# Kernel tuning notes

Measured on AMD Instinct MI355X. Metric: run time of the kernel, lower is better.

The kernel has to match this reference:

```python
import jax, jax.numpy as jnp
import numpy as np

DIMS = 512
NUM_HEADS = 8
KEY_DIM = DIMS // NUM_HEADS  # 64
VAL_DIM = DIMS               # 512, shared across heads
B, L = 4, 2048


def setup_inputs() -> dict:
    key = jax.random.key(0)
    ks = jax.random.split(key, 13)
    s = 0.02
    return {
        "query": jax.random.normal(ks[0], (B, L, DIMS), dtype=jnp.float32),
        "key": jax.random.normal(ks[1], (B, L, DIMS), dtype=jnp.float32),
        "value": jax.random.normal(ks[2], (B, L, DIMS), dtype=jnp.float32),
        # linear weights stored as (in, out)
        "Wq": jax.random.normal(ks[3], (DIMS, KEY_DIM * NUM_HEADS), dtype=jnp.float32) * s,
        "bq": jnp.zeros((KEY_DIM * NUM_HEADS,), dtype=jnp.float32),
        "Wk": jax.random.normal(ks[4], (DIMS, KEY_DIM * NUM_HEADS), dtype=jnp.float32) * s,
        "bk": jnp.zeros((KEY_DIM * NUM_HEADS,), dtype=jnp.float32),
        "Wv": jax.random.normal(ks[5], (DIMS, VAL_DIM), dtype=jnp.float32) * s,
        "bv": jnp.zeros((VAL_DIM,), dtype=jnp.float32),
        "Wo": jax.random.normal(ks[6], (VAL_DIM * NUM_HEADS, DIMS), dtype=jnp.float32) * s,
        "bo": jnp.zeros((DIMS,), dtype=jnp.float32),
    }


def reference(query, key, value, Wq, bq, Wk, bk, Wv, bv, Wo, bo):
    b, l, _ = query.shape
    m = key.shape[1]
    q = (query @ Wq + bq).reshape(b, l, KEY_DIM, NUM_HEADS)   # blkh
    k = (key @ Wk + bk).reshape(b, m, KEY_DIM, NUM_HEADS)     # bmkh
    v = value @ Wv + bv                                        # bmv (shared over heads)
    # causal mask: -inf strictly above the diagonal
    mask = jnp.where(jnp.arange(m)[None, :] > jnp.arange(l)[:, None],
                     jnp.float32(-jnp.inf), jnp.float32(0.0))  # [l, m]
    scores = jnp.einsum('blkh,bmkh->bhlm', q, k) + mask
    # original divides (scores+mask) by sqrt(key_dim) before softmax
    attn = jax.nn.softmax(scores / jnp.sqrt(jnp.float32(KEY_DIM)), axis=-1)
    vals = jnp.einsum('bhlm,bmv->blhv', attn, v).reshape(b, l, NUM_HEADS * VAL_DIM)
    return vals @ Wo + bo
```

## Files before the change

kernel.cpp:

```cpp
#include <hip/hip_runtime.h>
#include <hip/hip_bf16.h>


typedef __attribute__((ext_vector_type(8))) short bf16x8;
typedef __attribute__((ext_vector_type(4))) float f32x4;
typedef unsigned short u16;
typedef unsigned int u32;

#define DIMS  512
#define NHEAD 8
#define KDIM  64
#define VDIM  512
#define BATCH 4
#define SEQ   2048
#define ROWS  (BATCH * SEQ)
#define OCOLS (NHEAD * VDIM)

__device__ __forceinline__ u16 f2bf(float x) {
  __hip_bfloat16 b = __float2bfloat16(x);
  u16 u; __builtin_memcpy(&u, &b, 2); return u;
}
__device__ __forceinline__ float bf2f(u16 u) {
  __hip_bfloat16 b; __builtin_memcpy(&b, &u, 2); return __bfloat162float(b);
}

__global__ __launch_bounds__(256) void cast_bf16(
    const float* __restrict__ in, u16* __restrict__ out, int n8) {
  int i = blockIdx.x * 256 + threadIdx.x;
  if (i >= n8) return;
  const float4* p = reinterpret_cast<const float4*>(in) + (size_t)i * 2;
  float4 a0 = p[0], a1 = p[1];
  bf16x8 v;
  v[0] = f2bf(a0.x); v[1] = f2bf(a0.y); v[2] = f2bf(a0.z); v[3] = f2bf(a0.w);
  v[4] = f2bf(a1.x); v[5] = f2bf(a1.y); v[6] = f2bf(a1.z); v[7] = f2bf(a1.w);
  reinterpret_cast<bf16x8*>(out)[i] = v;
}

__global__ __launch_bounds__(256) void transpose_to_bf16(
    const float* __restrict__ in, u16* __restrict__ out, int R, int C) {
  __shared__ float t[32][33];
  int tx = threadIdx.x & 31, ty = threadIdx.x >> 5;
  int r0 = blockIdx.y * 32, c0 = blockIdx.x * 32;
  #pragma unroll
  for (int i = 0; i < 32; i += 8)
    t[ty + i][tx] = in[(size_t)(r0 + ty + i) * C + c0 + tx];
  __syncthreads();
  #pragma unroll
  for (int i = 0; i < 32; i += 8) {
    int oc = ty + i;
    out[(size_t)(c0 + oc) * R + r0 + tx] = f2bf(t[tx][oc]);
  }
}

__global__ __launch_bounds__(256) void proj_kernel(
    const u16* __restrict__ Xb, const u16* __restrict__ Wt,
    const float* __restrict__ bias, u16* __restrict__ out,
    int mode, float scale) {
  __shared__ u16 Ct[64][72];
  int lane = threadIdx.x & 63, wave = threadIdx.x >> 6;
  int g = lane >> 4, l15 = lane & 15;
  int row0 = blockIdx.y * 64, cb = blockIdx.x * 64;
  int gr = row0 + wave * 16 + l15;
  f32x4 acc[4] = {};
  for (int k0 = 0; k0 < DIMS; k0 += 32) {
    int ka = k0 + g * 8;
    bf16x8 a = *reinterpret_cast<const bf16x8*>(Xb + (size_t)gr * DIMS + ka);
    #pragma unroll
    for (int c = 0; c < 4; ++c) {
      bf16x8 bfr = *reinterpret_cast<const bf16x8*>(Wt + (size_t)(cb + c * 16 + l15) * DIMS + ka);
      acc[c] = __builtin_amdgcn_mfma_f32_16x16x32_bf16(a, bfr, acc[c], 0, 0, 0);
    }
  }
  #pragma unroll
  for (int c = 0; c < 4; ++c) {
    int col = c * 16 + l15;
    float bi = bias[cb + col];
    #pragma unroll
    for (int r = 0; r < 4; ++r) {
      int rl = wave * 16 + g * 4 + r;
      float v = (acc[c][r] + bi) * scale;
      if (mode == 0) Ct[rl][col] = f2bf(v);
      else           Ct[col][rl] = f2bf(v);
    }
  }
  __syncthreads();
  if (mode == 0) {
    int kd0 = cb >> 3;
    #pragma unroll
    for (int s2 = 0; s2 < 2; ++s2) {
      int seg = threadIdx.x + s2 * 256;
      int l = seg >> 3, h = seg & 7;
      bf16x8 vp;
      #pragma unroll
      for (int j = 0; j < 8; ++j) vp[j] = (short)Ct[l][h + 8 * j];
      int row = row0 + l;
      int b = row >> 11, ll = row & 2047;
      *reinterpret_cast<bf16x8*>(out + (((size_t)(b * NHEAD + h) * SEQ + ll) * KDIM + kd0)) = vp;
    }
  } else {
    int v_ = threadIdx.x >> 2, ch = threadIdx.x & 3;
    int b = row0 >> 11, m0 = row0 & 2047;
    bf16x8 p0, p1;
    #pragma unroll
    for (int j = 0; j < 8; ++j) { p0[j] = (short)Ct[v_][ch * 16 + j]; p1[j] = (short)Ct[v_][ch * 16 + 8 + j]; }
    u16* dst = out + ((size_t)(b * VDIM + cb + v_)) * SEQ + m0 + ch * 16;
    *reinterpret_cast<bf16x8*>(dst) = p0;
    *reinterpret_cast<bf16x8*>(dst + 8) = p1;
  }
}

__global__ __launch_bounds__(256, 3) void attn_kernel(
    const u16* __restrict__ Qp, const u16* __restrict__ Kp,
    const u16* __restrict__ Vt, u16* __restrict__ vals) {
  __shared__ char P[4][4096];
  int lane = threadIdx.x & 63, wave = threadIdx.x >> 6;
  int g = lane >> 4, l15 = lane & 15;
  int wg = blockIdx.x;
  int xcd = wg & 7, idx = wg >> 3;
  int bh = xcd * 4 + (idx & 3);
  int qt = 63 - (idx >> 2);
  int b = bh >> 3, h = bh & 7;
  int q0 = qt * 32;
  const u16* Qh = Qp + (size_t)bh * SEQ * KDIM;
  const u16* Kh = Kp + (size_t)bh * SEQ * KDIM;
  const u16* Vw = Vt + (size_t)b * VDIM * SEQ + (size_t)(wave * 128) * SEQ;
  char* Pw = P[wave];

  bf16x8 qb[2][2];
  #pragma unroll
  for (int rf = 0; rf < 2; ++rf)
    #pragma unroll
    for (int ks = 0; ks < 2; ++ks)
      qb[rf][ks] = *reinterpret_cast<const bf16x8*>(
          Qh + (size_t)(q0 + rf * 16 + l15) * KDIM + ks * 32 + g * 8);

  f32x4 acc[2][8] = {};
  float rs[2] = {0.f, 0.f};
  int nt = (qt >> 1) + 1;
  int nfull = (qt * 32 + 1) >> 6;

  auto tile = [&](int t, bool masked) {
    int m0 = t * 64;
    #pragma unroll
    for (int hf = 0; hf < 2; ++hf) {
      bf16x8 ka[2][2];
      #pragma unroll
      for (int i = 0; i < 2; ++i)
        #pragma unroll
        for (int ks = 0; ks < 2; ++ks)
          ka[i][ks] = *reinterpret_cast<const bf16x8*>(
              Kh + (size_t)(m0 + (hf * 2 + i) * 16 + l15) * KDIM + ks * 32 + g * 8);
      f32x4 st[2][2] = {};
      #pragma unroll
      for (int ks = 0; ks < 2; ++ks)
        #pragma unroll
        for (int i = 0; i < 2; ++i)
          #pragma unroll
          for (int rf = 0; rf < 2; ++rf)
            st[i][rf] = __builtin_amdgcn_mfma_f32_16x16x32_bf16(ka[i][ks], qb[rf][ks], st[i][rf], 0, 0, 0);
      #pragma unroll
      for (int i = 0; i < 2; ++i) {
        int mb = hf * 2 + i;
        int mbase = m0 + mb * 16 + g * 4;
        #pragma unroll
        for (int rf = 0; rf < 2; ++rf) {
          int qv = q0 + rf * 16 + l15;
          u16 pb[4];
          #pragma unroll
          for (int r = 0; r < 4; ++r) {
            float p = (masked && (mbase + r > qv)) ? 0.f : exp2f(st[i][rf][r]);
            pb[r] = f2bf(p);
            rs[rf] += bf2f(pb[r]);
          }
          uint2 w;
          w.x = (u32)pb[0] | ((u32)pb[1] << 16);
          w.y = (u32)pb[2] | ((u32)pb[3] << 16);
          int row = rf * 16 + l15;
          int byt = row * 128 + ((mb * 32 + g * 8) ^ ((row & 7) << 4));
          *reinterpret_cast<uint2*>(Pw + byt) = w;
        }
      }
    }
    #pragma unroll
    for (int ks = 0; ks < 2; ++ks) {
      bf16x8 pa[2];
      #pragma unroll
      for (int ar = 0; ar < 2; ++ar) {
        int row = ar * 16 + l15;
        pa[ar] = *reinterpret_cast<const bf16x8*>(
            Pw + row * 128 + ((ks * 64 + g * 16) ^ ((row & 7) << 4)));
      }
      #pragma unroll
      for (int c = 0; c < 8; ++c) {
        bf16x8 vb = *reinterpret_cast<const bf16x8*>(
            Vw + (size_t)(c * 16 + l15) * SEQ + m0 + ks * 32 + g * 8);
        #pragma unroll
        for (int ar = 0; ar < 2; ++ar)
          acc[ar][c] = __builtin_amdgcn_mfma_f32_16x16x32_bf16(pa[ar], vb, acc[ar][c], 0, 0, 0);
      }
    }
  };

  for (int t = 0; t < nfull; ++t) tile(t, false);
  for (int t = nfull; t < nt; ++t) tile(t, true);

  #pragma unroll
  for (int rf = 0; rf < 2; ++rf) {
    float v = rs[rf];
    v += __shfl_xor(v, 16);
    v += __shfl_xor(v, 32);
    rs[rf] = 1.0f / v;
  }
  float rinv[2][4];
  #pragma unroll
  for (int ar = 0; ar < 2; ++ar)
    #pragma unroll
    for (int r = 0; r < 4; ++r)
      rinv[ar][r] = __shfl(rs[ar], (lane & 48) | (((lane >> 4) & 3) * 4 + r));

  #pragma unroll
  for (int ar = 0; ar < 2; ++ar) {
    #pragma unroll
    for (int c = 0; c < 8; ++c) {
      int vcol = wave * 128 + c * 16 + l15;
      #pragma unroll
      for (int r = 0; r < 4; ++r) {
        int row = ar * 16 + g * 4 + r;
        float o = acc[ar][c][r] * rinv[ar][r];
        vals[((size_t)(b * SEQ + q0 + row)) * OCOLS + h * VDIM + vcol] = f2bf(o);
      }
    }
  }
}

__global__ __launch_bounds__(256) void out_gemm(
    const u16* __restrict__ vals, const u16* __restrict__ Wot,
    const float* __restrict__ bo, float* __restrict__ out) {
  __shared__ char As[128 * 128];
  __shared__ char Bs[64 * 128];
  int t = threadIdx.x;
  int lane = t & 63, wave = t >> 6;
  int g = lane >> 4, l15 = lane & 15;
  int id = (blockIdx.x & 7) * 64 + (blockIdx.x >> 3);
  int bx = id & 7, by = id >> 3;
  int row0 = by * 128, col0 = bx * 64;
  const int NT = OCOLS / 64;

  auto aglob = [&](int kt, int i) {
    int cid = t + i * 256, r = cid >> 3, ch = cid & 7;
    return *reinterpret_cast<const bf16x8*>(vals + (size_t)(row0 + r) * OCOLS + kt * 64 + ch * 8);
  };
  auto bglob = [&](int kt, int i) {
    int cid = t + i * 256, r = cid >> 3, ch = cid & 7;
    return *reinterpret_cast<const bf16x8*>(Wot + (size_t)(col0 + r) * OCOLS + kt * 64 + ch * 8);
  };
  auto stash = [&](bf16x8* av, bf16x8* bv) {
    #pragma unroll
    for (int i = 0; i < 4; ++i) {
      int cid = t + i * 256, r = cid >> 3, ch = cid & 7;
      *reinterpret_cast<bf16x8*>(As + r * 128 + ((ch * 16) ^ ((r & 7) << 4))) = av[i];
    }
    #pragma unroll
    for (int i = 0; i < 2; ++i) {
      int cid = t + i * 256, r = cid >> 3, ch = cid & 7;
      *reinterpret_cast<bf16x8*>(Bs + r * 128 + ((ch * 16) ^ ((r & 7) << 4))) = bv[i];
    }
  };

  f32x4 acc[2][4] = {};
  bf16x8 av[4], bv[2];
  #pragma unroll
  for (int i = 0; i < 4; ++i) av[i] = aglob(0, i);
  #pragma unroll
  for (int i = 0; i < 2; ++i) bv[i] = bglob(0, i);
  stash(av, bv);
  __syncthreads();

  for (int kt = 0; kt < NT; ++kt) {
    bf16x8 an[4], bn[2];
    if (kt + 1 < NT) {
      #pragma unroll
      for (int i = 0; i < 4; ++i) an[i] = aglob(kt + 1, i);
      #pragma unroll
      for (int i = 0; i < 2; ++i) bn[i] = bglob(kt + 1, i);
    }
    #pragma unroll
    for (int ks = 0; ks < 2; ++ks) {
      bf16x8 af[2];
      #pragma unroll
      for (int rf = 0; rf < 2; ++rf) {
        int row = wave * 32 + rf * 16 + l15;
        af[rf] = *reinterpret_cast<const bf16x8*>(As + row * 128 + ((ks * 64 + g * 16) ^ ((row & 7) << 4)));
      }
      #pragma unroll
      for (int c = 0; c < 4; ++c) {
        int row = c * 16 + l15;
        bf16x8 bfr = *reinterpret_cast<const bf16x8*>(Bs + row * 128 + ((ks * 64 + g * 16) ^ ((row & 7) << 4)));
        #pragma unroll
        for (int rf = 0; rf < 2; ++rf)
          acc[rf][c] = __builtin_amdgcn_mfma_f32_16x16x32_bf16(af[rf], bfr, acc[rf][c], 0, 0, 0);
      }
    }
    __syncthreads();
    if (kt + 1 < NT) {
      stash(an, bn);
      __syncthreads();
    }
  }

  #pragma unroll
  for (int c = 0; c < 4; ++c) {
    int col = col0 + c * 16 + l15;
    float bi = bo[col];
    #pragma unroll
    for (int rf = 0; rf < 2; ++rf)
      #pragma unroll
      for (int r = 0; r < 4; ++r) {
        int row = row0 + wave * 32 + rf * 16 + g * 4 + r;
        out[(size_t)row * DIMS + col] = acc[rf][c][r] + bi;
      }
  }
}

extern "C" void kernel_launch(void* const* d_in, const int* in_sizes, int n_in,
                              void* d_out, int out_size, void* d_ws, size_t ws_size,
                              hipStream_t stream) {
  const float* query = (const float*)d_in[0];
  const float* key   = (const float*)d_in[1];
  const float* value = (const float*)d_in[2];
  const float* Wq    = (const float*)d_in[3];
  const float* bq    = (const float*)d_in[4];
  const float* Wk    = (const float*)d_in[5];
  const float* bk    = (const float*)d_in[6];
  const float* Wv    = (const float*)d_in[7];
  const float* bv    = (const float*)d_in[8];
  const float* Wo    = (const float*)d_in[9];
  const float* bo    = (const float*)d_in[10];
  float* out = (float*)d_out;

  char* ws = (char*)d_ws;
  size_t off = 0;
  auto alloc = [&](size_t bytes) {
    char* p = ws + off; off += (bytes + 255) & ~(size_t)255; return p;
  };
  u16* Wqt  = (u16*)alloc((size_t)512 * 512 * 2);
  u16* Wkt  = (u16*)alloc((size_t)512 * 512 * 2);
  u16* Wvt  = (u16*)alloc((size_t)512 * 512 * 2);
  u16* Wot  = (u16*)alloc((size_t)512 * 4096 * 2);
  u16* Qp   = (u16*)alloc((size_t)BATCH * NHEAD * SEQ * KDIM * 2);
  u16* Kp   = (u16*)alloc((size_t)BATCH * NHEAD * SEQ * KDIM * 2);
  u16* Vt   = (u16*)alloc((size_t)BATCH * VDIM * SEQ * 2);
  u16* vals = (u16*)alloc((size_t)ROWS * OCOLS * 2);
  u16* Xq = vals;
  u16* Xk = vals + (size_t)ROWS * DIMS;
  u16* Xv = vals + (size_t)2 * ROWS * DIMS;

  dim3 tb(256);
  const int N8 = ROWS * DIMS / 8;
  cast_bf16<<<dim3(N8 / 256), tb, 0, stream>>>(query, Xq, N8);
  cast_bf16<<<dim3(N8 / 256), tb, 0, stream>>>(key,   Xk, N8);
  cast_bf16<<<dim3(N8 / 256), tb, 0, stream>>>(value, Xv, N8);

  transpose_to_bf16<<<dim3(16, 16), tb, 0, stream>>>(Wq, Wqt, 512, 512);
  transpose_to_bf16<<<dim3(16, 16), tb, 0, stream>>>(Wk, Wkt, 512, 512);
  transpose_to_bf16<<<dim3(16, 16), tb, 0, stream>>>(Wv, Wvt, 512, 512);
  transpose_to_bf16<<<dim3(16, 128), tb, 0, stream>>>(Wo, Wot, 4096, 512);

  const float qscale = 0.18033688011112042f;
  proj_kernel<<<dim3(8, 128), tb, 0, stream>>>(Xq, Wqt, bq, Qp, 0, qscale);
  proj_kernel<<<dim3(8, 128), tb, 0, stream>>>(Xk, Wkt, bk, Kp, 0, 1.0f);
  proj_kernel<<<dim3(8, 128), tb, 0, stream>>>(Xv, Wvt, bv, Vt, 2, 1.0f);

  attn_kernel<<<dim3(2048), tb, 0, stream>>>(Qp, Kp, Vt, vals);

  out_gemm<<<dim3(512), tb, 0, stream>>>(vals, Wot, bo, out);
}
```

Measured before the change: 676.6 us.

## Split QK score work across waves with shared P tile and prefetch

Previously every wave recomputed the full 32x64 score tile and exp for its own P copy. Now each wave computes only a 16-row key slice, the waves share a double-buffered P tile through LDS with a block barrier, and the row sums are combined across waves in shared memory. K for the next tile is prefetched, V loads are issued early, the fully masked parts of the last tile are skipped, and MFMA sections run at raised priority. This removes redundant QK and exp work at the cost of a __syncthreads per tile. Row sums are now taken from the fp32 probabilities rather than the rounded bf16 values.

Measured after the change: 746.2 us. +10.3%, slower.

```diff
diff --git a/kernel.cpp b/kernel.cpp
--- a/kernel.cpp
+++ b/kernel.cpp
@@ -19,9 +19,6 @@
 __device__ __forceinline__ u16 f2bf(float x) {
   __hip_bfloat16 b = __float2bfloat16(x);
   u16 u; __builtin_memcpy(&u, &b, 2); return u;
-}
-__device__ __forceinline__ float bf2f(u16 u) {
-  __hip_bfloat16 b; __builtin_memcpy(&b, &u, 2); return __bfloat162float(b);
 }
 
 __global__ __launch_bounds__(256) void cast_bf16(
@@ -112,7 +109,9 @@
 __global__ __launch_bounds__(256, 3) void attn_kernel(
     const u16* __restrict__ Qp, const u16* __restrict__ Kp,
     const u16* __restrict__ Vt, u16* __restrict__ vals) {
-  __shared__ char P[4][4096];
+  __shared__ char Pb[2][4096];
+  __shared__ float Lpart[4][32];
+  __shared__ float Rinv[32];
   int lane = threadIdx.x & 63, wave = threadIdx.x >> 6;
   int g = lane >> 4, l15 = lane & 15;
   int wg = blockIdx.x;
@@ -124,7 +123,6 @@
   const u16* Qh = Qp + (size_t)bh * SEQ * KDIM;
   const u16* Kh = Kp + (size_t)bh * SEQ * KDIM;
   const u16* Vw = Vt + (size_t)b * VDIM * SEQ + (size_t)(wave * 128) * SEQ;
-  char* Pw = P[wave];
 
   bf16x8 qb[2][2];
   #pragma unroll
@@ -137,86 +135,114 @@
   f32x4 acc[2][8] = {};
   float rs[2] = {0.f, 0.f};
   int nt = (qt >> 1) + 1;
-  int nfull = (qt * 32 + 1) >> 6;
-
-  auto tile = [&](int t, bool masked) {
-    int m0 = t * 64;
-    #pragma unroll
-    for (int hf = 0; hf < 2; ++hf) {
-      bf16x8 ka[2][2];
-      #pragma unroll
-      for (int i = 0; i < 2; ++i)
-        #pragma unroll
-        for (int ks = 0; ks < 2; ++ks)
-          ka[i][ks] = *reinterpret_cast<const bf16x8*>(
-              Kh + (size_t)(m0 + (hf * 2 + i) * 16 + l15) * KDIM + ks * 32 + g * 8);
-      f32x4 st[2][2] = {};
+  int mrow = wave * 16 + l15;
+
+  bf16x8 ka[2], kan[2];
+  #pragma unroll
+  for (int ks = 0; ks < 2; ++ks)
+    ka[ks] = *reinterpret_cast<const bf16x8*>(Kh + (size_t)mrow * KDIM + ks * 32 + g * 8);
+
+  for (int t = 0; t < nt; ++t) {
+    const int m0 = t * 64;
+    const bool masked = (t == nt - 1);
+    const bool live = !masked || (m0 + wave * 16 <= q0 + 31);
+    const bool chunk1 = !masked || (m0 + 32 <= q0 + 31);
+    char* P = Pb[t & 1];
+
+    bf16x8 v0[8];
+    #pragma unroll
+    for (int c = 0; c < 8; ++c)
+      v0[c] = *reinterpret_cast<const bf16x8*>(Vw + (size_t)(c * 16 + l15) * SEQ + m0 + g * 8);
+
+    f32x4 st[2] = {};
+    if (live) {
       #pragma unroll
       for (int ks = 0; ks < 2; ++ks)
         #pragma unroll
-        for (int i = 0; i < 2; ++i)
-          #pragma unroll
-          for (int rf = 0; rf < 2; ++rf)
-            st[i][rf] = __builtin_amdgcn_mfma_f32_16x16x32_bf16(ka[i][ks], qb[rf][ks], st[i][rf], 0, 0, 0);
-      #pragma unroll
-      for (int i = 0; i < 2; ++i) {
-        int mb = hf * 2 + i;
-        int mbase = m0 + mb * 16 + g * 4;
+        for (int rf = 0; rf < 2; ++rf)
+          st[rf] = __builtin_amdgcn_mfma_f32_16x16x32_bf16(ka[ks], qb[rf][ks], st[rf], 0, 0, 0);
+    }
+
+    if (t + 1 < nt) {
+      #pragma unroll
+      for (int ks = 0; ks < 2; ++ks)
+        kan[ks] = *reinterpret_cast<const bf16x8*>(
+            Kh + (size_t)((t + 1) * 64 + mrow) * KDIM + ks * 32 + g * 8);
+    }
+
+    if (live) {
+      #pragma unroll
+      for (int rf = 0; rf < 2; ++rf) {
+        int qv_off = q0 + rf * 16 + l15 - (m0 + wave * 16 + g * 4);
+        u16 pb[4];
         #pragma unroll
-        for (int rf = 0; rf < 2; ++rf) {
-          int qv = q0 + rf * 16 + l15;
-          u16 pb[4];
-          #pragma unroll
-          for (int r = 0; r < 4; ++r) {
-            float p = (masked && (mbase + r > qv)) ? 0.f : exp2f(st[i][rf][r]);
-            pb[r] = f2bf(p);
-            rs[rf] += bf2f(pb[r]);
-          }
-          uint2 w;
-          w.x = (u32)pb[0] | ((u32)pb[1] << 16);
-          w.y = (u32)pb[2] | ((u32)pb[3] << 16);
-          int row = rf * 16 + l15;
-          int byt = row * 128 + ((mb * 32 + g * 8) ^ ((row & 7) << 4));
-          *reinterpret_cast<uint2*>(Pw + byt) = w;
+        for (int r = 0; r < 4; ++r) {
+          float p = (masked && r > qv_off) ? 0.f : exp2f(st[rf][r]);
+          pb[r] = f2bf(p);
+          rs[rf] += p;
         }
-      }
-    }
-    #pragma unroll
-    for (int ks = 0; ks < 2; ++ks) {
-      bf16x8 pa[2];
+        uint2 w;
+        w.x = (u32)pb[0] | ((u32)pb[1] << 16);
+        w.y = (u32)pb[2] | ((u32)pb[3] << 16);
+        int ql = rf * 16 + l15;
+        *reinterpret_cast<uint2*>(P + ql * 128 + ((32 * wave + 8 * g) ^ ((ql & 7) << 4))) = w;
+      }
+    }
+    __syncthreads();
+
+    bf16x8 v1[8];
+    if (chunk1) {
+      #pragma unroll
+      for (int c = 0; c < 8; ++c)
+        v1[c] = *reinterpret_cast<const bf16x8*>(Vw + (size_t)(c * 16 + l15) * SEQ + m0 + 32 + g * 8);
+    }
+
+    bf16x8 pa[2];
+    #pragma unroll
+    for (int ar = 0; ar < 2; ++ar) {
+      int qr = ar * 16 + l15;
+      pa[ar] = *reinterpret_cast<const bf16x8*>(P + qr * 128 + ((g * 16) ^ ((qr & 7) << 4)));
+    }
+    __builtin_amdgcn_s_setprio(1);
+    #pragma unroll
+    for (int c = 0; c < 8; ++c)
+      #pragma unroll
+      for (int ar = 0; ar < 2; ++ar)
+        acc[ar][c] = __builtin_amdgcn_mfma_f32_16x16x32_bf16(pa[ar], v0[c], acc[ar][c], 0, 0, 0);
+    __builtin_amdgcn_s_setprio(0);
+    if (chunk1) {
       #pragma unroll
       for (int ar = 0; ar < 2; ++ar) {
-        int row = ar * 16 + l15;
-        pa[ar] = *reinterpret_cast<const bf16x8*>(
-            Pw + row * 128 + ((ks * 64 + g * 16) ^ ((row & 7) << 4)));
-      }
-      #pragma unroll
-      for (int c = 0; c < 8; ++c) {
-        bf16x8 vb = *reinterpret_cast<const bf16x8*>(
-            Vw + (size_t)(c * 16 + l15) * SEQ + m0 + ks * 32 + g * 8);
+        int qr = ar * 16 + l15;
+        pa[ar] = *reinterpret_cast<const bf16x8*>(P + qr * 128 + ((64 + g * 16) ^ ((qr & 7) << 4)));
+      }
+      __builtin_amdgcn_s_setprio(1);
+      #pragma unroll
+      for (int c = 0; c < 8; ++c)
         #pragma unroll
         for (int ar = 0; ar < 2; ++ar)
-          acc[ar][c] = __builtin_amdgcn_mfma_f32_16x16x32_bf16(pa[ar], vb, acc[ar][c], 0, 0, 0);
-      }
-    }
-  };
-
-  for (int t = 0; t < nfull; ++t) tile(t, false);
-  for (int t = nfull; t < nt; ++t) tile(t, true);
+          acc[ar][c] = __builtin_amdgcn_mfma_f32_16x16x32_bf16(pa[ar], v1[c], acc[ar][c], 0, 0, 0);
+      __builtin_amdgcn_s_setprio(0);
+    }
+    ka[0] = kan[0]; ka[1] = kan[1];
+  }
 
   #pragma unroll
   for (int rf = 0; rf < 2; ++rf) {
     float v = rs[rf];
     v += __shfl_xor(v, 16);
     v += __shfl_xor(v, 32);
-    rs[rf] = 1.0f / v;
-  }
-  float rinv[2][4];
-  #pragma unroll
-  for (int ar = 0; ar < 2; ++ar)
-    #pragma unroll
-    for (int r = 0; r < 4; ++r)
-      rinv[ar][r] = __shfl(rs[ar], (lane & 48) | (((lane >> 4) & 3) * 4 + r));
+    rs[rf] = v;
+  }
+  if (lane < 16) {
+    Lpart[wave][lane] = rs[0];
+    Lpart[wave][16 + lane] = rs[1];
+  }
+  __syncthreads();
+  if (threadIdx.x < 32)
+    Rinv[threadIdx.x] = 1.0f / (Lpart[0][threadIdx.x] + Lpart[1][threadIdx.x] +
+                                Lpart[2][threadIdx.x] + Lpart[3][threadIdx.x]);
+  __syncthreads();
 
   #pragma unroll
   for (int ar = 0; ar < 2; ++ar) {
@@ -226,7 +252,7 @@
       #pragma unroll
       for (int r = 0; r < 4; ++r) {
         int row = ar * 16 + g * 4 + r;
-        float o = acc[ar][c][r] * rinv[ar][r];
+        float o = acc[ar][c][r] * Rinv[row];
         vals[((size_t)(b * SEQ + q0 + row)) * OCOLS + h * VDIM + vcol] = f2bf(o);
       }
     }
```

## Share QK^T score tile across waves via double-buffered LDS and pipeline next tile

Applied to the files above, without the earlier changes.

Previously each of the four waves recomputed the full 32x64 score tile (QK^T and exp) redundantly and kept its own P buffer. Now each wave computes only its own 16-column slice of scores, writes it into a shared double-buffered LDS P tile, and the next tile's K load and score phase overlap with the current PV MFMAs, separated by one barrier per tile. Row sums are combined across waves through LDS at the end, and the masking check is now applied to every tile instead of only the diagonal ones. This removes four-fold redundant score work but adds a block-wide barrier per tile and sums unrounded p values rather than bf16-rounded ones.

Measured after the change: 604.6 us. 10.7% less time.

```diff
diff --git a/kernel.cpp b/kernel.cpp
--- a/kernel.cpp
+++ b/kernel.cpp
@@ -19,9 +19,6 @@
 __device__ __forceinline__ u16 f2bf(float x) {
   __hip_bfloat16 b = __float2bfloat16(x);
   u16 u; __builtin_memcpy(&u, &b, 2); return u;
-}
-__device__ __forceinline__ float bf2f(u16 u) {
-  __hip_bfloat16 b; __builtin_memcpy(&b, &u, 2); return __bfloat162float(b);
 }
 
 __global__ __launch_bounds__(256) void cast_bf16(
@@ -112,7 +109,9 @@
 __global__ __launch_bounds__(256, 3) void attn_kernel(
     const u16* __restrict__ Qp, const u16* __restrict__ Kp,
     const u16* __restrict__ Vt, u16* __restrict__ vals) {
-  __shared__ char P[4][4096];
+  __shared__ u16 Plds[2][32 * 64];
+  __shared__ float Lpart[4][32];
+  __shared__ float Rinv[32];
   int lane = threadIdx.x & 63, wave = threadIdx.x >> 6;
   int g = lane >> 4, l15 = lane & 15;
   int wg = blockIdx.x;
@@ -124,99 +123,99 @@
   const u16* Qh = Qp + (size_t)bh * SEQ * KDIM;
   const u16* Kh = Kp + (size_t)bh * SEQ * KDIM;
   const u16* Vw = Vt + (size_t)b * VDIM * SEQ + (size_t)(wave * 128) * SEQ;
-  char* Pw = P[wave];
-
-  bf16x8 qb[2][2];
+
+  bf16x8 qa[2][2];
   #pragma unroll
   for (int rf = 0; rf < 2; ++rf)
     #pragma unroll
     for (int ks = 0; ks < 2; ++ks)
-      qb[rf][ks] = *reinterpret_cast<const bf16x8*>(
+      qa[rf][ks] = *reinterpret_cast<const bf16x8*>(
           Qh + (size_t)(q0 + rf * 16 + l15) * KDIM + ks * 32 + g * 8);
 
   f32x4 acc[2][8] = {};
-  float rs[2] = {0.f, 0.f};
+  float rs[2][4] = {};
   int nt = (qt >> 1) + 1;
-  int nfull = (qt * 32 + 1) >> 6;
-
-  auto tile = [&](int t, bool masked) {
+  int pcol = wave * 16 + l15;
+
+  auto kload = [&](int t, bf16x8* kb) {
+    const u16* base = Kh + (size_t)(t * 64 + wave * 16 + l15) * KDIM;
+    kb[0] = *reinterpret_cast<const bf16x8*>(base + g * 8);
+    kb[1] = *reinterpret_cast<const bf16x8*>(base + 32 + g * 8);
+  };
+  auto sphase = [&](int t, bf16x8 kb0, bf16x8 kb1) {
     int m0 = t * 64;
-    #pragma unroll
-    for (int hf = 0; hf < 2; ++hf) {
-      bf16x8 ka[2][2];
-      #pragma unroll
-      for (int i = 0; i < 2; ++i)
-        #pragma unroll
-        for (int ks = 0; ks < 2; ++ks)
-          ka[i][ks] = *reinterpret_cast<const bf16x8*>(
-              Kh + (size_t)(m0 + (hf * 2 + i) * 16 + l15) * KDIM + ks * 32 + g * 8);
-      f32x4 st[2][2] = {};
-      #pragma unroll
-      for (int ks = 0; ks < 2; ++ks)
-        #pragma unroll
-        for (int i = 0; i < 2; ++i)
-          #pragma unroll
-          for (int rf = 0; rf < 2; ++rf)
-            st[i][rf] = __builtin_amdgcn_mfma_f32_16x16x32_bf16(ka[i][ks], qb[rf][ks], st[i][rf], 0, 0, 0);
-      #pragma unroll
-      for (int i = 0; i < 2; ++i) {
-        int mb = hf * 2 + i;
-        int mbase = m0 + mb * 16 + g * 4;
-        #pragma unroll
-        for (int rf = 0; rf < 2; ++rf) {
-          int qv = q0 + rf * 16 + l15;
-          u16 pb[4];
-          #pragma unroll
-          for (int r = 0; r < 4; ++r) {
-            float p = (masked && (mbase + r > qv)) ? 0.f : exp2f(st[i][rf][r]);
-            pb[r] = f2bf(p);
-            rs[rf] += bf2f(pb[r]);
-          }
-          uint2 w;
-          w.x = (u32)pb[0] | ((u32)pb[1] << 16);
-          w.y = (u32)pb[2] | ((u32)pb[3] << 16);
-          int row = rf * 16 + l15;
-          int byt = row * 128 + ((mb * 32 + g * 8) ^ ((row & 7) << 4));
-          *reinterpret_cast<uint2*>(Pw + byt) = w;
-        }
-      }
-    }
+    u16* P = Plds[t & 1];
+    f32x4 s[2] = {};
+    #pragma unroll
+    for (int rf = 0; rf < 2; ++rf) {
+      s[rf] = __builtin_amdgcn_mfma_f32_16x16x32_bf16(qa[rf][0], kb0, s[rf], 0, 0, 0);
+      s[rf] = __builtin_amdgcn_mfma_f32_16x16x32_bf16(qa[rf][1], kb1, s[rf], 0, 0, 0);
+    }
+    #pragma unroll
+    for (int rf = 0; rf < 2; ++rf)
+      #pragma unroll
+      for (int r = 0; r < 4; ++r) {
+        int prow = rf * 16 + g * 4 + r;
+        float p = (m0 + pcol > q0 + prow) ? 0.f : exp2f(s[rf][r]);
+        rs[rf][r] += p;
+        P[prow * 64 + (pcol ^ ((prow & 7) << 3))] = f2bf(p);
+      }
+  };
+
+  { bf16x8 kb[2]; kload(0, kb); sphase(0, kb[0], kb[1]); }
+  __syncthreads();
+
+  for (int t = 0; t < nt; ++t) {
+    int m0 = t * 64;
+    const u16* P = Plds[t & 1];
+    bool more = (t + 1 < nt);
+    bf16x8 kb[2];
+    if (more) kload(t + 1, kb);
     #pragma unroll
     for (int ks = 0; ks < 2; ++ks) {
+      bf16x8 vb[8];
+      #pragma unroll
+      for (int c = 0; c < 8; ++c)
+        vb[c] = *reinterpret_cast<const bf16x8*>(
+            Vw + (size_t)(c * 16 + l15) * SEQ + m0 + ks * 32 + g * 8);
       bf16x8 pa[2];
       #pragma unroll
       for (int ar = 0; ar < 2; ++ar) {
-        int row = ar * 16 + l15;
+        int qr = ar * 16 + l15;
         pa[ar] = *reinterpret_cast<const bf16x8*>(
-            Pw + row * 128 + ((ks * 64 + g * 16) ^ ((row & 7) << 4)));
-      }
-      #pragma unroll
-      for (int c = 0; c < 8; ++c) {
-        bf16x8 vb = *reinterpret_cast<const bf16x8*>(
-            Vw + (size_t)(c * 16 + l15) * SEQ + m0 + ks * 32 + g * 8);
+            &P[qr * 64 + ((ks * 32 + g * 8) ^ ((qr & 7) << 3))]);
+      }
+      #pragma unroll
+      for (int c = 0; c < 8; ++c)
         #pragma unroll
         for (int ar = 0; ar < 2; ++ar)
-          acc[ar][c] = __builtin_amdgcn_mfma_f32_16x16x32_bf16(pa[ar], vb, acc[ar][c], 0, 0, 0);
-      }
-    }
-  };
-
-  for (int t = 0; t < nfull; ++t) tile(t, false);
-  for (int t = nfull; t < nt; ++t) tile(t, true);
-
-  #pragma unroll
-  for (int rf = 0; rf < 2; ++rf) {
-    float v = rs[rf];
-    v += __shfl_xor(v, 16);
-    v += __shfl_xor(v, 32);
-    rs[rf] = 1.0f / v;
-  }
-  float rinv[2][4];
-  #pragma unroll
-  for (int ar = 0; ar < 2; ++ar)
-    #pragma unroll
-    for (int r = 0; r < 4; ++r)
-      rinv[ar][r] = __shfl(rs[ar], (lane & 48) | (((lane >> 4) & 3) * 4 + r));
+          acc[ar][c] = __builtin_amdgcn_mfma_f32_16x16x32_bf16(pa[ar], vb[c], acc[ar][c], 0, 0, 0);
+    }
+    if (more) sphase(t + 1, kb[0], kb[1]);
+    __syncthreads();
+  }
+
+  #pragma unroll
+  for (int rf = 0; rf < 2; ++rf)
+    #pragma unroll
+    for (int r = 0; r < 4; ++r) {
+      float v = rs[rf][r];
+      v += __shfl_xor(v, 1); v += __shfl_xor(v, 2);
+      v += __shfl_xor(v, 4); v += __shfl_xor(v, 8);
+      rs[rf][r] = v;
+    }
+  if (l15 == 0) {
+    #pragma unroll
+    for (int rf = 0; rf < 2; ++rf)
+      #pragma unroll
+      for (int r = 0; r < 4; ++r)
+        Lpart[wave][rf * 16 + g * 4 + r] = rs[rf][r];
+  }
+  __syncthreads();
+  if (threadIdx.x < 32)
+    Rinv[threadIdx.x] = 1.0f / (Lpart[0][threadIdx.x] + Lpart[1][threadIdx.x] +
+                                Lpart[2][threadIdx.x] + Lpart[3][threadIdx.x]);
+  __syncthreads();
 
   #pragma unroll
   for (int ar = 0; ar < 2; ++ar) {
@@ -226,7 +225,7 @@
       #pragma unroll
       for (int r = 0; r < 4; ++r) {
         int row = ar * 16 + g * 4 + r;
-        float o = acc[ar][c][r] * rinv[ar][r];
+        float o = acc[ar][c][r] * Rinv[row];
         vals[((size_t)(b * SEQ + q0 + row)) * OCOLS + h * VDIM + vcol] = f2bf(o);
       }
     }
```
